# Optimization experiments

Hardware: AMD Instinct MI355X
Metric: run time of the kernel (lower is better)

The kernel has to match this reference:

```python
import jax, jax.numpy as jnp
import numpy as np

B, T, D = 32, 512, 768      # batch, n_tokens, input_dim
M, K, R = 2048, 32, 128     # n_mentions, k_retrieval, retrieval_dim
H = 1024                    # hidden_dim
EPS = 1e-12


def _layer_norm(x, scale, bias, eps=EPS):
    mu = jnp.mean(x, axis=-1, keepdims=True)
    var = jnp.mean(jnp.square(x - mu), axis=-1, keepdims=True)
    return (x - mu) * jax.lax.rsqrt(var + eps) * scale + bias


def _mlp_block(x, w1, b1, w2, b2, ln_s, ln_b):
    # Dense -> gelu -> Dense -> residual -> LayerNorm (dropout off, deterministic)
    h = jax.nn.gelu(x @ w1 + b1)
    h = h @ w2 + b2
    return _layer_norm(h + x, ln_s, ln_b)


def setup_inputs() -> dict:
    key = jax.random.key(0)
    ks = jax.random.split(key, 24)
    s = lambda *sh: 1.0 / np.sqrt(sh[0])
    inp = {
        'encoded_input': jax.random.normal(ks[0], (B, T, D), jnp.float32),
        'retrieval_values': jax.random.normal(ks[1], (M, K, R), jnp.float32),
        'retrieval_scores': jax.random.uniform(ks[2], (M, K), jnp.float32),
        'mention_batch_positions': jax.random.randint(ks[3], (M,), 0, B),
        'mention_start_positions': jax.random.randint(ks[4], (M,), 0, T),
        'mention_end_positions': jax.random.randint(ks[5], (M,), 0, T),
        'mention_mask': jnp.ones((M,), jnp.float32),
        # value_projection: concat(start,end) [2D] -> R
        'vp_w': jax.random.normal(ks[6], (2 * D, R), jnp.float32) * s(2 * D),
        'vp_b': jnp.zeros((R,), jnp.float32),
        # concat_mlp: [2R] -> H ; concat_dense: H -> D
        'cm_w': jax.random.normal(ks[7], (2 * R, H), jnp.float32) * s(2 * R),
        'cm_b': jnp.zeros((H,), jnp.float32),
        'cd_w': jax.random.normal(ks[8], (H, D), jnp.float32) * s(H),
        'cd_b': jnp.zeros((D,), jnp.float32),
        # additional concat MLPBlock (1 layer)
        'ac_w1': jax.random.normal(ks[9], (D, H), jnp.float32) * s(D),
        'ac_b1': jnp.zeros((H,), jnp.float32),
        'ac_w2': jax.random.normal(ks[10], (H, D), jnp.float32) * s(H),
        'ac_b2': jnp.zeros((D,), jnp.float32),
        'ac_ln_s': jnp.ones((D,), jnp.float32),
        'ac_ln_b': jnp.zeros((D,), jnp.float32),
        # pooled MLPBlock (1 layer)
        'pl_w1': jax.random.normal(ks[11], (D, H), jnp.float32) * s(D),
        'pl_b1': jnp.zeros((H,), jnp.float32),
        'pl_w2': jax.random.normal(ks[12], (H, D), jnp.float32) * s(H),
        'pl_b2': jnp.zeros((D,), jnp.float32),
        'pl_ln_s': jnp.ones((D,), jnp.float32),
        'pl_ln_b': jnp.zeros((D,), jnp.float32),
        # final layer norm
        'ln_s': jnp.ones((D,), jnp.float32),
        'ln_b': jnp.zeros((D,), jnp.float32),
    }
    return inp


def reference(encoded_input, retrieval_values, retrieval_scores,
              mention_batch_positions, mention_start_positions,
              mention_end_positions, mention_mask,
              vp_w, vp_b, cm_w, cm_b, cd_w, cd_b,
              ac_w1, ac_b1, ac_w2, ac_b2, ac_ln_s, ac_ln_b,
              pl_w1, pl_b1, pl_w2, pl_b2, pl_ln_s, pl_ln_b,
              ln_s, ln_b):
    # gather mention start/end encodings: [M, D] each
    start_enc = encoded_input[mention_batch_positions, mention_start_positions]
    end_enc = encoded_input[mention_batch_positions, mention_end_positions]
    pmv = jnp.concatenate((start_enc, end_enc), axis=-1) @ vp_w + vp_b  # [M, R]
    # tile over retrievals and concat: [M, K, 2R]
    pmv = jnp.broadcast_to(pmv[:, None, :], (pmv.shape[0], retrieval_values.shape[1], pmv.shape[-1]))
    cv = jnp.concatenate((pmv, retrieval_values), axis=-1)
    cv = jax.nn.gelu(cv @ cm_w + cm_b)
    cv = cv @ cd_w + cd_b                                              # [M, K, D]
    cv = _mlp_block(cv, ac_w1, ac_b1, ac_w2, ac_b2, ac_ln_s, ac_ln_b)
    pooled = jnp.einsum('qk,qkd->qd', retrieval_scores, cv)            # [M, D]
    pooled = _mlp_block(pooled, pl_w1, pl_b1, pl_w2, pl_b2, pl_ln_s, pl_ln_b)
    pooled = pooled * mention_mask[:, None]
    out = encoded_input.at[mention_batch_positions, mention_start_positions].add(pooled)
    return _layer_norm(out, ln_s, ln_b)
```

## Files before the change

### kernel.cpp

```cpp
#include <hip/hip_runtime.h>
#include <hip/hip_bf16.h>

#define Bq 32
#define Tq 512
#define Dq 768
#define Mq 2048
#define Kq 32
#define Rq 128
#define Hq 1024
#define NROWS (Mq * Kq)
#define CH 16384
#define NCH (NROWS / CH)

typedef short short8 __attribute__((ext_vector_type(8)));
typedef unsigned short ushort4v __attribute__((ext_vector_type(4)));
typedef float f32x4 __attribute__((ext_vector_type(4)));

__device__ __forceinline__ unsigned short f2bf(float f) {
    union { float f; unsigned u; } v; v.f = f;
    unsigned r = v.u + 0x7FFFu + ((v.u >> 16) & 1u);
    return (unsigned short)(r >> 16);
}
__device__ __forceinline__ float bf2f(unsigned short h) {
    union { unsigned u; float f; } v; v.u = ((unsigned)h) << 16;
    return v.f;
}
__device__ __forceinline__ float gelu_f(float x) {
    float u = x * (1.5957691216057308f + 0.07135481622212034f * x * x);
    return x / (1.0f + __expf(-u));
}

__device__ __forceinline__ void block_reduce2(float& a, float& b, float* sm) {
    #pragma unroll
    for (int off = 32; off > 0; off >>= 1) {
        a += __shfl_down(a, off, 64);
        b += __shfl_down(b, off, 64);
    }
    int lane = threadIdx.x & 63, wid = threadIdx.x >> 6;
    if (lane == 0) { sm[wid * 2] = a; sm[wid * 2 + 1] = b; }
    __syncthreads();
    if (threadIdx.x == 0) {
        float sa = 0.f, sb = 0.f;
        #pragma unroll
        for (int w = 0; w < 4; ++w) { sa += sm[w * 2]; sb += sm[w * 2 + 1]; }
        sm[0] = sa; sm[1] = sb;
    }
    __syncthreads();
    a = sm[0]; b = sm[1];
    __syncthreads();
}

__global__ __launch_bounds__(256) void wtrans_k(
    const float* __restrict__ W, unsigned short* __restrict__ Wt, int K, int N)
{
    __shared__ unsigned short t[32][33];
    int n0 = blockIdx.x * 32, k0 = blockIdx.y * 32;
    int tx = threadIdx.x & 31, ty = threadIdx.x >> 5;
    #pragma unroll
    for (int i = 0; i < 32; i += 8)
        t[ty + i][tx] = f2bf(W[(long)(k0 + ty + i) * N + n0 + tx]);
    __syncthreads();
    #pragma unroll
    for (int i = 0; i < 32; i += 8)
        Wt[(long)(n0 + ty + i) * K + k0 + tx] = t[tx][ty + i];
}

__global__ __launch_bounds__(256) void rv2bf_k(
    const float* __restrict__ rv, unsigned short* __restrict__ rvb)
{
    long i = ((long)blockIdx.x * 256 + threadIdx.x) * 8;
    float4 a = *reinterpret_cast<const float4*>(rv + i);
    float4 b = *reinterpret_cast<const float4*>(rv + i + 4);
    unsigned short v[8] = {f2bf(a.x), f2bf(a.y), f2bf(a.z), f2bf(a.w),
                           f2bf(b.x), f2bf(b.y), f2bf(b.z), f2bf(b.w)};
    *(short8*)(rvb + i) = *(short8*)v;
}

__global__ __launch_bounds__(192) void gather_enc_k(
    const float* __restrict__ enc, const int* __restrict__ bpos,
    const int* __restrict__ spos, const int* __restrict__ epos,
    unsigned short* __restrict__ cat)
{
    int m = blockIdx.x;
    int t = threadIdx.x;
    int b = bpos[m];
    int pos = (t < 96) ? spos[m] : epos[m];
    int off = (t < 96) ? t * 8 : (t - 96) * 8;
    const float4* s = reinterpret_cast<const float4*>(enc + ((long)b * Tq + pos) * Dq + off);
    float4 a = s[0], c = s[1];
    unsigned short v[8] = {f2bf(a.x), f2bf(a.y), f2bf(a.z), f2bf(a.w),
                           f2bf(c.x), f2bf(c.y), f2bf(c.z), f2bf(c.w)};
    *(short8*)(cat + (long)m * 1536 + t * 8) = *(short8*)v;
}

template <int ACT, int OUT_BF16, int RESID, int CONCAT>
__global__ __launch_bounds__(256) void mgemm_k(
    const unsigned short* __restrict__ A,
    const unsigned short* __restrict__ Wt,
    const float* __restrict__ bias,
    void* __restrict__ Cout,
    const unsigned short* __restrict__ resid,
    int Kd, int N,
    const unsigned short* __restrict__ pmvb,
    const unsigned short* __restrict__ rvb,
    int row_base)
{
    __shared__ __align__(16) unsigned short AsLin[2][128 * 32];
    __shared__ __align__(16) unsigned short BsLin[2][128 * 32];
    const int tid = threadIdx.x;
    const int w = tid >> 6, lane = tid & 63;
    const int wr = w >> 1, wc = w & 1;
    const int lr = lane & 15, lk = lane >> 4;
    const long r0 = (long)blockIdx.x * 128;
    const int c0 = blockIdx.y * 128;
    const int nt = Kd >> 5;

    auto stage = [&](int buf, int t) {
        const int k0 = t << 5;
        #pragma unroll
        for (int cc = 0; cc < 2; ++cc) {
            int idx = (w * 2 + cc) * 64 + lane;
            int row = idx >> 2, kc = idx & 3;
            int kcol = k0 + kc * 8;
            const unsigned short* ga;
            if (CONCAT) {
                long gr = row_base + r0 + row;
                ga = (kcol < 128) ? pmvb + ((gr >> 5) << 7) + kcol
                                  : rvb + (gr << 7) + (kcol - 128);
            } else {
                ga = A + (r0 + row) * Kd + kcol;
            }
            __builtin_amdgcn_global_load_lds(
                (const __attribute__((address_space(1))) void*)ga,
                (__attribute__((address_space(3))) void*)(&AsLin[buf][(w * 2 + cc) * 512]),
                16, 0, 0);
            const unsigned short* gb = Wt + (long)(c0 + row) * Kd + kcol;
            __builtin_amdgcn_global_load_lds(
                (const __attribute__((address_space(1))) void*)gb,
                (__attribute__((address_space(3))) void*)(&BsLin[buf][(w * 2 + cc) * 512]),
                16, 0, 0);
        }
    };

    f32x4 acc[4][4] = {};

    stage(0, 0);
    if (nt > 1) stage(1, 1);

    for (int t = 0; t < nt; ++t) {
        const int cur = t & 1;
        if (t + 1 < nt) asm volatile("s_waitcnt vmcnt(4)" ::: "memory");
        else            asm volatile("s_waitcnt vmcnt(0)" ::: "memory");
        asm volatile("s_barrier" ::: "memory");

        short8 af[4], bv[4];
        #pragma unroll
        for (int m = 0; m < 4; ++m)
            af[m] = *(const short8*)(&AsLin[cur][(wr * 64 + m * 16 + lr) * 32 + lk * 8]);
        #pragma unroll
        for (int n = 0; n < 4; ++n)
            bv[n] = *(const short8*)(&BsLin[cur][(wc * 64 + n * 16 + lr) * 32 + lk * 8]);

        asm volatile("s_waitcnt lgkmcnt(0)" ::: "memory");
        asm volatile("s_barrier" ::: "memory");

        if (t + 2 < nt) stage(cur, t + 2);

        #pragma unroll
        for (int m = 0; m < 4; ++m)
            #pragma unroll
            for (int n = 0; n < 4; ++n)
                acc[m][n] = __builtin_amdgcn_mfma_f32_16x16x32_bf16(
                    af[m], bv[n], acc[m][n], 0, 0, 0);
    }

    const int cb = c0 + wc * 64;
    #pragma unroll
    for (int n = 0; n < 4; ++n) {
        const int c = cb + n * 16 + lr;
        const float bc = bias[c];
        #pragma unroll
        for (int m = 0; m < 4; ++m) {
            const long r = r0 + wr * 64 + m * 16 + lk * 4;
            #pragma unroll
            for (int j = 0; j < 4; ++j) {
                float v = acc[m][n][j] + bc;
                if (ACT) v = gelu_f(v);
                if (RESID) v += bf2f(resid[(r + j) * N + c]);
                if (OUT_BF16) ((unsigned short*)Cout)[(r + j) * N + c] = f2bf(v);
                else          ((float*)Cout)[(r + j) * N + c] = v;
            }
        }
    }
}

__global__ __launch_bounds__(512) void ln_pool_part_k(
    const unsigned short* __restrict__ cvb, const float* __restrict__ scores,
    const float* __restrict__ ln_s, const float* __restrict__ ln_b,
    float* __restrict__ partial,
    int mbase)
{
    __shared__ float part[8][768];
    int lm = blockIdx.x >> 2, ks = blockIdx.x & 3;
    int gm = mbase + lm;
    int tid = threadIdx.x, lane = tid & 63, wid = tid >> 6;
    int k = ks * 8 + wid;
    const unsigned short* row = cvb + ((long)lm * 32 + k) * Dq;

    float v[12], gs[12], gb[12];
    float s = 0.f, ss = 0.f;
    #pragma unroll
    for (int j = 0; j < 3; ++j) {
        int col = j * 256 + lane * 4;
        ushort4v u = *(const ushort4v*)(row + col);
        float4 g = *reinterpret_cast<const float4*>(ln_s + col);
        float4 h = *reinterpret_cast<const float4*>(ln_b + col);
        #pragma unroll
        for (int t = 0; t < 4; ++t) {
            float x = bf2f(u[t]);
            v[j * 4 + t] = x;
            s += x; ss += x * x;
        }
        gs[j * 4 + 0] = g.x; gs[j * 4 + 1] = g.y; gs[j * 4 + 2] = g.z; gs[j * 4 + 3] = g.w;
        gb[j * 4 + 0] = h.x; gb[j * 4 + 1] = h.y; gb[j * 4 + 2] = h.z; gb[j * 4 + 3] = h.w;
    }
    #pragma unroll
    for (int off = 32; off > 0; off >>= 1) {
        s  += __shfl_xor(s, off, 64);
        ss += __shfl_xor(ss, off, 64);
    }
    float mu = s * (1.0f / Dq);
    float var = ss * (1.0f / Dq) - mu * mu;
    float rstd = rsqrtf(var + 1e-12f);
    float sc = scores[gm * 32 + k];
    #pragma unroll
    for (int j = 0; j < 3; ++j) {
        int col = j * 256 + lane * 4;
        #pragma unroll
        for (int t = 0; t < 4; ++t)
            part[wid][col + t] = sc * ((v[j * 4 + t] - mu) * rstd * gs[j * 4 + t] + gb[j * 4 + t]);
    }
    __syncthreads();
    for (int d = tid; d < Dq; d += 512) {
        float acc = 0.f;
        #pragma unroll
        for (int w = 0; w < 8; ++w) acc += part[w][d];
        partial[((long)lm * 4 + ks) * Dq + d] = acc;
    }
}

__global__ __launch_bounds__(256) void ln_pool_comb_k(
    const float* __restrict__ partial, float* __restrict__ pooledf,
    unsigned short* __restrict__ pooledb, int mbase)
{
    int lm = blockIdx.x, gm = mbase + lm;
    int tid = threadIdx.x;
    for (int d = tid; d < Dq; d += 256) {
        const float* p = partial + (long)lm * 4 * Dq + d;
        float s = p[0] + p[Dq] + p[2 * Dq] + p[3 * Dq];
        pooledf[(long)gm * Dq + d] = s;
        pooledb[(long)gm * Dq + d] = f2bf(s);
    }
}

__global__ __launch_bounds__(256) void ln_mask_scatter_k(
    const float* __restrict__ pu, const float* __restrict__ pooled,
    const float* __restrict__ ln_s, const float* __restrict__ ln_b,
    const float* __restrict__ mask,
    const int* __restrict__ bpos, const int* __restrict__ spos,
    float* __restrict__ out)
{
    __shared__ float sm[8];
    int m = blockIdx.x;
    int tid = threadIdx.x;
    float v[3];
    float s = 0.f, ss = 0.f;
    #pragma unroll
    for (int j = 0; j < 3; ++j) {
        int d = tid + j * 256;
        v[j] = pu[(long)m * Dq + d] + pooled[(long)m * Dq + d];
        s += v[j]; ss += v[j] * v[j];
    }
    block_reduce2(s, ss, sm);
    float mu = s * (1.0f / Dq);
    float var = ss * (1.0f / Dq) - mu * mu;
    float rstd = rsqrtf(var + 1e-12f);
    float mk = mask[m];
    long orow = ((long)bpos[m] * Tq + spos[m]) * Dq;
    #pragma unroll
    for (int j = 0; j < 3; ++j) {
        int d = tid + j * 256;
        float y = ((v[j] - mu) * rstd * ln_s[d] + ln_b[d]) * mk;
        atomicAdd(&out[orow + d], y);
    }
}

__global__ __launch_bounds__(256) void final_ln_k(
    float* __restrict__ out, const float* __restrict__ ln_s,
    const float* __restrict__ ln_b)
{
    __shared__ float sm[8];
    int tid = threadIdx.x;
    float* row = out + (long)blockIdx.x * Dq;
    float v[3];
    float s = 0.f, ss = 0.f;
    #pragma unroll
    for (int j = 0; j < 3; ++j) {
        v[j] = row[tid + j * 256];
        s += v[j]; ss += v[j] * v[j];
    }
    block_reduce2(s, ss, sm);
    float mu = s * (1.0f / Dq);
    float var = ss * (1.0f / Dq) - mu * mu;
    float rstd = rsqrtf(var + 1e-12f);
    #pragma unroll
    for (int j = 0; j < 3; ++j) {
        int d = tid + j * 256;
        row[d] = (v[j] - mu) * rstd * ln_s[d] + ln_b[d];
    }
}

extern "C" void kernel_launch(void* const* d_in, const int* in_sizes, int n_in,
                              void* d_out, int out_size, void* d_ws, size_t ws_size,
                              hipStream_t stream) {
    const float* enc    = (const float*)d_in[0];
    const float* rv     = (const float*)d_in[1];
    const float* scores = (const float*)d_in[2];
    const int*   bpos   = (const int*)d_in[3];
    const int*   spos   = (const int*)d_in[4];
    const int*   epos   = (const int*)d_in[5];
    const float* mask   = (const float*)d_in[6];
    const float* vp_w   = (const float*)d_in[7];
    const float* vp_b   = (const float*)d_in[8];
    const float* cm_w   = (const float*)d_in[9];
    const float* cm_b   = (const float*)d_in[10];
    const float* cd_w   = (const float*)d_in[11];
    const float* cd_b   = (const float*)d_in[12];
    const float* ac_w1  = (const float*)d_in[13];
    const float* ac_b1  = (const float*)d_in[14];
    const float* ac_w2  = (const float*)d_in[15];
    const float* ac_b2  = (const float*)d_in[16];
    const float* ac_ln_s = (const float*)d_in[17];
    const float* ac_ln_b = (const float*)d_in[18];
    const float* pl_w1  = (const float*)d_in[19];
    const float* pl_b1  = (const float*)d_in[20];
    const float* pl_w2  = (const float*)d_in[21];
    const float* pl_b2  = (const float*)d_in[22];
    const float* pl_ln_s = (const float*)d_in[23];
    const float* pl_ln_b = (const float*)d_in[24];
    const float* ln_s   = (const float*)d_in[25];
    const float* ln_b   = (const float*)d_in[26];
    float* out = (float*)d_out;

    char* wsb = (char*)d_ws;
    unsigned short* wt_cm = (unsigned short*)wsb; wsb += (size_t)1024 * 256 * 2;
    unsigned short* wt_cd = (unsigned short*)wsb; wsb += (size_t)768 * 1024 * 2;
    unsigned short* wt_a1 = (unsigned short*)wsb; wsb += (size_t)1024 * 768 * 2;
    unsigned short* wt_a2 = (unsigned short*)wsb; wsb += (size_t)768 * 1024 * 2;
    unsigned short* wt_p1 = (unsigned short*)wsb; wsb += (size_t)1024 * 768 * 2;
    unsigned short* wt_p2 = (unsigned short*)wsb; wsb += (size_t)768 * 1024 * 2;
    unsigned short* wt_vp = (unsigned short*)wsb; wsb += (size_t)128 * 1536 * 2;
    unsigned short* pmvb  = (unsigned short*)wsb; wsb += (size_t)Mq * Rq * 2;
    unsigned short* rvb   = (unsigned short*)wsb; wsb += (size_t)NROWS * Rq * 2;
    unsigned short* catenc = (unsigned short*)wsb; wsb += (size_t)Mq * 1536 * 2;
    unsigned short* hb    = (unsigned short*)wsb; wsb += (size_t)CH * Hq * 2;
    unsigned short* tb    = (unsigned short*)wsb; wsb += (size_t)CH * Dq * 2;
    unsigned short* cvb   = (unsigned short*)wsb; wsb += (size_t)CH * Dq * 2;
    float* partial = (float*)wsb; wsb += (size_t)(CH / Kq) * 4 * Dq * 4;
    float* pooledf = (float*)wsb; wsb += (size_t)Mq * Dq * 4;
    unsigned short* pooledb = (unsigned short*)wsb; wsb += (size_t)Mq * Dq * 2;
    float* puf     = (float*)wsb; wsb += (size_t)Mq * Dq * 4;

    hipMemcpyAsync(out, enc, (size_t)Bq * Tq * Dq * sizeof(float),
                   hipMemcpyDeviceToDevice, stream);

    wtrans_k<<<dim3(1024 / 32, 256 / 32), 256, 0, stream>>>(cm_w, wt_cm, 256, 1024);
    wtrans_k<<<dim3(768 / 32, 1024 / 32), 256, 0, stream>>>(cd_w, wt_cd, 1024, 768);
    wtrans_k<<<dim3(1024 / 32, 768 / 32), 256, 0, stream>>>(ac_w1, wt_a1, 768, 1024);
    wtrans_k<<<dim3(768 / 32, 1024 / 32), 256, 0, stream>>>(ac_w2, wt_a2, 1024, 768);
    wtrans_k<<<dim3(1024 / 32, 768 / 32), 256, 0, stream>>>(pl_w1, wt_p1, 768, 1024);
    wtrans_k<<<dim3(768 / 32, 1024 / 32), 256, 0, stream>>>(pl_w2, wt_p2, 1024, 768);
    wtrans_k<<<dim3(128 / 32, 1536 / 32), 256, 0, stream>>>(vp_w, wt_vp, 1536, 128);
    rv2bf_k<<<(NROWS * Rq) / (256 * 8), 256, 0, stream>>>(rv, rvb);

    gather_enc_k<<<Mq, 192, 0, stream>>>(enc, bpos, spos, epos, catenc);
    mgemm_k<0, 1, 0, 0><<<dim3(Mq / 128, 1), 256, 0, stream>>>(
        catenc, wt_vp, vp_b, pmvb, nullptr, 1536, Rq, nullptr, nullptr, 0);

    for (int c = 0; c < NCH; ++c) {
        int row_base = c * CH;
        int mbase = c * (CH / Kq);
        mgemm_k<1, 1, 0, 1><<<dim3(CH / 128, Hq / 128), 256, 0, stream>>>(
            nullptr, wt_cm, cm_b, hb, nullptr, 2 * Rq, Hq, pmvb, rvb, row_base);
        mgemm_k<0, 1, 0, 0><<<dim3(CH / 128, Dq / 128), 256, 0, stream>>>(
            hb, wt_cd, cd_b, tb, nullptr, Hq, Dq, nullptr, nullptr, 0);
        mgemm_k<1, 1, 0, 0><<<dim3(CH / 128, Hq / 128), 256, 0, stream>>>(
            tb, wt_a1, ac_b1, hb, nullptr, Dq, Hq, nullptr, nullptr, 0);
        mgemm_k<0, 1, 1, 0><<<dim3(CH / 128, Dq / 128), 256, 0, stream>>>(
            hb, wt_a2, ac_b2, cvb, tb, Hq, Dq, nullptr, nullptr, 0);
        ln_pool_part_k<<<(CH / Kq) * 4, 512, 0, stream>>>(
            cvb, scores, ac_ln_s, ac_ln_b, partial, mbase);
        ln_pool_comb_k<<<CH / Kq, 256, 0, stream>>>(partial, pooledf, pooledb, mbase);
    }

    mgemm_k<1, 1, 0, 0><<<dim3(Mq / 128, Hq / 128), 256, 0, stream>>>(
        pooledb, wt_p1, pl_b1, hb, nullptr, Dq, Hq, nullptr, nullptr, 0);
    mgemm_k<0, 0, 0, 0><<<dim3(Mq / 128, Dq / 128), 256, 0, stream>>>(
        hb, wt_p2, pl_b2, puf, nullptr, Hq, Dq, nullptr, nullptr, 0);

    ln_mask_scatter_k<<<Mq, 256, 0, stream>>>(puf, pooledf, pl_ln_s, pl_ln_b,
                                              mask, bpos, spos, out);

    final_ln_k<<<Bq * Tq, 256, 0, stream>>>(out, ln_s, ln_b);
}
```

Measured before the change: 792.3 us.

## Add 256-row block GEMM kernel with larger per-wave tiles for chunk MLP

Introduces a 512-thread GEMM kernel computing 256x256 or 256x192 output tiles, with each wave owning a 128-row slab, and uses it for the four per-chunk GEMMs. It also doubles the chunk size so fewer chunk iterations are launched. Larger tiles raise arithmetic intensity and cut redundant global and LDS traffic for A and B, at the cost of higher register pressure (128 accumulator registers), lower occupancy, and larger intermediate buffers.

```diff
diff --git a/kernel.cpp b/kernel.cpp
--- a/kernel.cpp
+++ b/kernel.cpp
@@ -9,7 +9,7 @@
 #define Rq 128
 #define Hq 1024
 #define NROWS (Mq * Kq)
-#define CH 16384
+#define CH 32768
 #define NCH (NROWS / CH)
 
 typedef short short8 __attribute__((ext_vector_type(8)));
@@ -182,6 +182,110 @@
         #pragma unroll
         for (int m = 0; m < 4; ++m) {
             const long r = r0 + wr * 64 + m * 16 + lk * 4;
+            #pragma unroll
+            for (int j = 0; j < 4; ++j) {
+                float v = acc[m][n][j] + bc;
+                if (ACT) v = gelu_f(v);
+                if (RESID) v += bf2f(resid[(r + j) * N + c]);
+                if (OUT_BF16) ((unsigned short*)Cout)[(r + j) * N + c] = f2bf(v);
+                else          ((float*)Cout)[(r + j) * N + c] = v;
+            }
+        }
+    }
+}
+
+template <int ACT, int OUT_BF16, int RESID, int CONCAT, int NF>
+__global__ __launch_bounds__(512, 2) void mgemm256_k(
+    const unsigned short* __restrict__ A,
+    const unsigned short* __restrict__ Wt,
+    const float* __restrict__ bias,
+    void* __restrict__ Cout,
+    const unsigned short* __restrict__ resid,
+    int Kd, int N,
+    const unsigned short* __restrict__ pmvb,
+    const unsigned short* __restrict__ rvb,
+    int row_base)
+{
+    __shared__ __align__(16) unsigned short As[2][256 * 32];
+    __shared__ __align__(16) unsigned short Bs[2][NF * 64 * 32];
+    const int tid = threadIdx.x;
+    const int w = tid >> 6, lane = tid & 63;
+    const int wr = w >> 2, wc = w & 3;
+    const int lr = lane & 15, lk = lane >> 4;
+    const long r0 = (long)blockIdx.x * 256;
+    const int c0 = blockIdx.y * (NF * 64);
+    const int nt = Kd >> 5;
+    const int wb = (NF == 4) ? w : (w >= 6 ? w - 6 : w);
+
+    auto stage = [&](int buf, int t) {
+        const int k0 = t << 5;
+        #pragma unroll
+        for (int q = 0; q < 2; ++q) {
+            int ca = w * 128 + q * 64 + lane;
+            int rowa = ca >> 2, kca = ca & 3;
+            int kcol = k0 + kca * 8;
+            const unsigned short* ga;
+            if (CONCAT) {
+                long gr = row_base + r0 + rowa;
+                ga = (kcol < 128) ? pmvb + ((gr >> 5) << 7) + kcol
+                                  : rvb + (gr << 7) + (kcol - 128);
+            } else {
+                ga = A + (r0 + rowa) * Kd + kcol;
+            }
+            __builtin_amdgcn_global_load_lds(
+                (const __attribute__((address_space(1))) void*)ga,
+                (__attribute__((address_space(3))) void*)(&As[buf][(w * 128 + q * 64) * 8]),
+                16, 0, 0);
+            int cb_ = wb * 128 + q * 64 + lane;
+            int rowb = cb_ >> 2, kcb = cb_ & 3;
+            const unsigned short* gb = Wt + (long)(c0 + rowb) * Kd + k0 + kcb * 8;
+            __builtin_amdgcn_global_load_lds(
+                (const __attribute__((address_space(1))) void*)gb,
+                (__attribute__((address_space(3))) void*)(&Bs[buf][(wb * 128 + q * 64) * 8]),
+                16, 0, 0);
+        }
+    };
+
+    f32x4 acc[8][NF] = {};
+
+    stage(0, 0);
+    if (nt > 1) stage(1, 1);
+
+    for (int t = 0; t < nt; ++t) {
+        const int cur = t & 1;
+        if (t + 1 < nt) asm volatile("s_waitcnt vmcnt(4)" ::: "memory");
+        else            asm volatile("s_waitcnt vmcnt(0)" ::: "memory");
+        asm volatile("s_barrier" ::: "memory");
+
+        short8 af[8], bv[NF];
+        #pragma unroll
+        for (int m = 0; m < 8; ++m)
+            af[m] = *(const short8*)(&As[cur][(wr * 128 + m * 16 + lr) * 32 + lk * 8]);
+        #pragma unroll
+        for (int n = 0; n < NF; ++n)
+            bv[n] = *(const short8*)(&Bs[cur][(wc * (NF * 16) + n * 16 + lr) * 32 + lk * 8]);
+
+        asm volatile("s_waitcnt lgkmcnt(0)" ::: "memory");
+        asm volatile("s_barrier" ::: "memory");
+
+        if (t + 2 < nt) stage(cur, t + 2);
+
+        #pragma unroll
+        for (int m = 0; m < 8; ++m)
+            #pragma unroll
+            for (int n = 0; n < NF; ++n)
+                acc[m][n] = __builtin_amdgcn_mfma_f32_16x16x32_bf16(
+                    af[m], bv[n], acc[m][n], 0, 0, 0);
+    }
+
+    const int cb = c0 + wc * (NF * 16);
+    #pragma unroll
+    for (int n = 0; n < NF; ++n) {
+        const int c = cb + n * 16 + lr;
+        const float bc = bias[c];
+        #pragma unroll
+        for (int m = 0; m < 8; ++m) {
+            const long r = r0 + wr * 128 + m * 16 + lk * 4;
             #pragma unroll
             for (int j = 0; j < 4; ++j) {
                 float v = acc[m][n][j] + bc;
@@ -390,13 +494,13 @@
     for (int c = 0; c < NCH; ++c) {
         int row_base = c * CH;
         int mbase = c * (CH / Kq);
-        mgemm_k<1, 1, 0, 1><<<dim3(CH / 128, Hq / 128), 256, 0, stream>>>(
+        mgemm256_k<1, 1, 0, 1, 4><<<dim3(CH / 256, Hq / 256), 512, 0, stream>>>(
             nullptr, wt_cm, cm_b, hb, nullptr, 2 * Rq, Hq, pmvb, rvb, row_base);
-        mgemm_k<0, 1, 0, 0><<<dim3(CH / 128, Dq / 128), 256, 0, stream>>>(
+        mgemm256_k<0, 1, 0, 0, 3><<<dim3(CH / 256, Dq / 192), 512, 0, stream>>>(
             hb, wt_cd, cd_b, tb, nullptr, Hq, Dq, nullptr, nullptr, 0);
-        mgemm_k<1, 1, 0, 0><<<dim3(CH / 128, Hq / 128), 256, 0, stream>>>(
+        mgemm256_k<1, 1, 0, 0, 4><<<dim3(CH / 256, Hq / 256), 512, 0, stream>>>(
             tb, wt_a1, ac_b1, hb, nullptr, Dq, Hq, nullptr, nullptr, 0);
-        mgemm_k<0, 1, 1, 0><<<dim3(CH / 128, Dq / 128), 256, 0, stream>>>(
+        mgemm256_k<0, 1, 1, 0, 3><<<dim3(CH / 256, Dq / 192), 512, 0, stream>>>(
             hb, wt_a2, ac_b2, cvb, tb, Hq, Dq, nullptr, nullptr, 0);
         ln_pool_part_k<<<(CH / Kq) * 4, 512, 0, stream>>>(
             cvb, scores, ac_ln_s, ac_ln_b, partial, mbase);
```

Measured after the change: 795.1 us. No clear change (+0.4%).
